# Optimization experiments

Measured on AMD Instinct MI355X. Metric: run time of the kernel, lower is better.

## Reference

```python
import jax, jax.numpy as jnp
import numpy as np

PI = float(np.pi)
TWO_PI = 2.0 * PI
LOG_2PI = float(np.log(TWO_PI))
N_FFT = 1024
LOG_N = 10
N_MAX = min(N_FFT, 2000)  # evaluate_z term cap


def _bitrev_indices(N, num_bits):
    idx = np.arange(N)
    rev = np.zeros(N, dtype=np.int32)
    v = idx.copy()
    for _ in range(num_bits):
        rev = (rev << 1) | (v & 1)
        v >>= 1
    return rev

_BITREV = jnp.asarray(_bitrev_indices(N_FFT, LOG_N))


def fft_fused(x_re, x_im):
    """Radix-2 DIT FFT with bit-reversal load, mirroring the Triton kernel.
    x_re/x_im: [B, N]. Returns (y_re, y_im)."""
    B, N = x_re.shape
    y = (x_re + 1j * x_im).astype(jnp.complex64)[:, _BITREV]
    for stage in range(LOG_N):
        s = 1 << stage          # half butterfly size (stride)
        # twiddles W_k = exp(-2*pi*i*k/(2s)), k in [0, s)
        k = jnp.arange(s)
        w = jnp.exp((-TWO_PI * 1j / (2 * s)) * k).astype(jnp.complex64)
        yg = y.reshape(B, N // (2 * s), 2, s)
        upper = yg[:, :, 0, :]
        lower = yg[:, :, 1, :] * w  # broadcast over [B, groups, s]
        y = jnp.concatenate([upper + lower, upper - lower], axis=-1).reshape(B, N)
    return jnp.real(y), jnp.imag(y)


def evaluate_z(t):
    """Riemann-Siegel Z(t) cosine sum with dynamic term count, masked."""
    t_half = t * 0.5
    theta = t_half * (jnp.log(t) - LOG_2PI) - t_half - PI / 8.0
    theta = theta + 1.0 / (48.0 * t)
    n = jnp.arange(1, N_MAX + 1, dtype=t.dtype)
    log_n = jnp.log(n)
    rsqrt_n = jax.lax.rsqrt(n)
    # [P, N_MAX] outer product of phases
    phases = t[:, None] * log_n[None, :] - theta[:, None]
    terms = rsqrt_n[None, :] * jnp.cos(phases)
    n_terms = jnp.clip(jnp.sqrt(jax.lax.stop_gradient(t) / TWO_PI).astype(jnp.int32), 10, N_MAX)
    mask = jnp.arange(N_MAX)[None, :] < n_terms[:, None]
    return 2.0 * jnp.sum(jnp.where(mask, terms, 0.0), axis=-1)


def setup_inputs() -> dict:
    key = jax.random.key(0)
    k1, k2, k3 = jax.random.split(key, 3)
    x_re = jax.random.normal(k1, (16384, N_FFT), dtype=jnp.float32)
    x_im = jax.random.normal(k2, (16384, N_FFT), dtype=jnp.float32)
    # evaluation points t in [1000, 101000)
    t = 1000.0 + 100000.0 * jax.random.uniform(k3, (262144,), dtype=jnp.float32)
    return {"x_re": x_re, "x_im": x_im, "t": t}


def reference(x_re, x_im, t):
    y_re, y_im = fft_fused(x_re, x_im)
    Z = evaluate_z(t)
    return (y_re, y_im, Z)
```

## Files before the change

### kernel.cpp

```cpp
#include <hip/hip_runtime.h>
#include <math.h>

#define INV_2PI_D 0.15915494309189535

#define LDSYNC() asm volatile("s_waitcnt lgkmcnt(0)" ::: "memory")

__device__ __forceinline__ int pad(int e) { return e + (e >> 4); }

__device__ __forceinline__ void bfly(float& ar, float& ai, float& br, float& bi,
                                     float wr, float wi) {
    const float tr = wr * br - wi * bi;
    const float ti = wr * bi + wi * br;
    br = ar - tr; bi = ai - ti;
    ar = ar + tr; ai = ai + ti;
}

__device__ __forceinline__ void wrev(float rev, float& c, float& s) {
    s = __builtin_amdgcn_sinf(rev);
    c = __builtin_amdgcn_cosf(rev);
}

__device__ __forceinline__ void fft_row(
    const float* __restrict__ xre, const float* __restrict__ xim,
    float* __restrict__ yre, float* __restrict__ yim,
    float* __restrict__ s,
    int row)
{
    const int lane = (int)(threadIdx.x & 63u);
    const size_t base = (size_t)row << 10;

    float re[16], im[16];

    const int rev6l = (int)(__brev((unsigned)lane) >> 26);
    const int REV4[16] = {0,8,4,12,2,10,6,14,1,9,5,13,3,11,7,15};
#pragma unroll
    for (int r = 0; r < 16; ++r) {
        const int a = REV4[r] * 64 + rev6l;
        re[r] = xre[base + a];
        im[r] = xim[base + a];
    }

    const int lo = lane & 15;
    const int hi = (lane >> 4) << 8;
    const float lof = (float)lo;

    float c8a[8], s8a[8];
#pragma unroll
    for (int m = 0; m < 8; ++m)
        wrev(-(16.0f * (float)m + lof) * (1.0f / 256.0f), c8a[m], s8a[m]);
    float c4a[4], s4a[4];
#pragma unroll
    for (int m = 0; m < 4; ++m)
        wrev(-(16.0f * (float)m + lof) * (1.0f / 128.0f), c4a[m], s4a[m]);
    float c2a[2], s2a[2];
#pragma unroll
    for (int m = 0; m < 2; ++m)
        wrev(-(16.0f * (float)m + lof) * (1.0f / 64.0f), c2a[m], s2a[m]);
    float c1a, s1a;
    wrev(-lof * (1.0f / 32.0f), c1a, s1a);

    const float W8R[8] = {1.f, 0.9238795325112867f, 0.7071067811865476f,
                          0.3826834323650898f, 0.f, -0.3826834323650898f,
                          -0.7071067811865476f, -0.9238795325112867f};
    const float W8I[8] = {0.f, -0.3826834323650898f, -0.7071067811865476f,
                          -0.9238795325112867f, -1.f, -0.9238795325112867f,
                          -0.7071067811865476f, -0.3826834323650898f};
#pragma unroll
    for (int st = 0; st < 4; ++st) {
        const int S = 1 << st;
#pragma unroll
        for (int rl = 0; rl < 16; ++rl) {
            if (rl & S) continue;
            const int k8 = (rl & (S - 1)) * (8 >> st);
            bfly(re[rl], im[rl], re[rl | S], im[rl | S], W8R[k8], W8I[k8]);
        }
    }

#pragma unroll
    for (int r = 0; r < 16; ++r) s[pad(lane * 16 + r)] = re[r];
    LDSYNC();
#pragma unroll
    for (int r = 0; r < 16; ++r) re[r] = s[pad(hi + (r << 4) + lo)];
    LDSYNC();
#pragma unroll
    for (int r = 0; r < 16; ++r) s[pad(lane * 16 + r)] = im[r];
    LDSYNC();
#pragma unroll
    for (int r = 0; r < 16; ++r) im[r] = s[pad(hi + (r << 4) + lo)];
    LDSYNC();

#pragma unroll
    for (int rl = 0; rl < 16; ++rl) if (!(rl & 1))
        bfly(re[rl], im[rl], re[rl|1], im[rl|1], c1a, s1a);
#pragma unroll
    for (int rl = 0; rl < 16; ++rl) if (!(rl & 2))
        bfly(re[rl], im[rl], re[rl|2], im[rl|2], c2a[rl & 1], s2a[rl & 1]);
#pragma unroll
    for (int rl = 0; rl < 16; ++rl) if (!(rl & 4))
        bfly(re[rl], im[rl], re[rl|4], im[rl|4], c4a[rl & 3], s4a[rl & 3]);
#pragma unroll
    for (int rl = 0; rl < 16; ++rl) if (!(rl & 8))
        bfly(re[rl], im[rl], re[rl|8], im[rl|8], c8a[rl & 7], s8a[rl & 7]);

    const float lf = (float)lane;
    float cz8[8], sz8[8];
#pragma unroll
    for (int m = 0; m < 8; ++m)
        wrev(-(64.0f * (float)m + lf) * (1.0f / 1024.0f), cz8[m], sz8[m]);
    float cz4[4], sz4[4];
#pragma unroll
    for (int m = 0; m < 4; ++m)
        wrev(-(64.0f * (float)m + lf) * (1.0f / 512.0f), cz4[m], sz4[m]);

#pragma unroll
    for (int r = 0; r < 16; ++r) s[pad(hi + (r << 4) + lo)] = re[r];
    LDSYNC();
#pragma unroll
    for (int r = 0; r < 16; ++r) re[r] = s[pad((r << 6) + lane)];
    LDSYNC();
#pragma unroll
    for (int r = 0; r < 16; ++r) s[pad(hi + (r << 4) + lo)] = im[r];
    LDSYNC();
#pragma unroll
    for (int r = 0; r < 16; ++r) im[r] = s[pad((r << 6) + lane)];
    LDSYNC();

#pragma unroll
    for (int rl = 0; rl < 16; ++rl) if (!(rl & 4))
        bfly(re[rl], im[rl], re[rl|4], im[rl|4], cz4[rl & 3], sz4[rl & 3]);
#pragma unroll
    for (int rl = 0; rl < 16; ++rl) if (!(rl & 8))
        bfly(re[rl], im[rl], re[rl|8], im[rl|8], cz8[rl & 7], sz8[rl & 7]);

#pragma unroll
    for (int r = 0; r < 16; ++r) {
        yre[base + (r << 6) + lane] = re[r];
        yim[base + (r << 6) + lane] = im[r];
    }
}

__global__ __launch_bounds__(256) void table_kernel(float* __restrict__ ws) {
    const int i = (int)(blockIdx.x * 256 + threadIdx.x);
    if (i < 1024) {
        const double nd = (double)(i + 1);
        ws[i]        = (float)log(nd);
        ws[1024 + i] = (float)(1.0 / sqrt(nd));
    }
}

__device__ void z_eval(const float* __restrict__ tin, float* __restrict__ zout,
                       const float* __restrict__ ws, int zblock, int n,
                       float* __restrict__ buf)
{
    for (int i = (int)threadIdx.x; i < 512; i += 256)
        reinterpret_cast<float4*>(buf)[i] = reinterpret_cast<const float4*>(ws)[i];
    __syncthreads();
    const float* slog = buf;
    const float* srsq = buf + 1024;

    const int gid = zblock * 256 + (int)threadIdx.x;
    if (gid >= n) return;

    const float t  = tin[gid];
    const float th = __fmul_rn(t, 0.5f);
    const float logt = (float)log((double)t);
    float theta = __fsub_rn(__fsub_rn(__fmul_rn(th, __fsub_rn(logt, 1.8378770664093453f)), th),
                            0.39269908169872414f);
    theta = __fadd_rn(theta, __fdiv_rn(1.0f, __fmul_rn(48.0f, t)));

    int nt = (int)sqrtf(__fdiv_rn(t, 6.283185307179586f));
    nt = min(max(nt, 10), 1024);

    float acc = 0.0f;
    for (int i = 0; i < nt; ++i) {
        const float p = __fsub_rn(__fmul_rn(t, slog[i]), theta);
        const double rev = (double)p * INV_2PI_D;
        const double fr  = rev - rint(rev);
        const float  c   = __builtin_amdgcn_cosf((float)fr);
        acc = __fmaf_rn(srsq[i], c, acc);
    }
    zout[gid] = __fmul_rn(2.0f, acc);
}

__global__ __launch_bounds__(256, 6) void fused_kernel(
    const float* __restrict__ xre, const float* __restrict__ xim,
    const float* __restrict__ tin, const float* __restrict__ ws,
    float* __restrict__ yre, float* __restrict__ yim, float* __restrict__ zout,
    int z_blocks, int nrows, int nz)
{
    __shared__ float s[4][1088];

    const int b = (int)blockIdx.x;
    if (b < z_blocks) {
        z_eval(tin, zout, ws, b, nz, &s[0][0]);
    } else {
        const int wid = (int)(threadIdx.x >> 6);
        const int row = ((b - z_blocks) << 2) | wid;
        if (row < nrows)
            fft_row(xre, xim, yre, yim, s[wid], row);
    }
}

extern "C" void kernel_launch(void* const* d_in, const int* in_sizes, int n_in,
                              void* d_out, int out_size, void* d_ws, size_t ws_size,
                              hipStream_t stream)
{
    const float* xre = (const float*)d_in[0];
    const float* xim = (const float*)d_in[1];
    const float* t   = (const float*)d_in[2];

    const size_t nfft = (size_t)in_sizes[0];
    const int nrows = (int)(nfft >> 10);
    const int nz    = in_sizes[2];

    float* yre = (float*)d_out;
    float* yim = yre + nfft;
    float* z   = yre + 2 * nfft;
    float* ws  = (float*)d_ws;

    table_kernel<<<4, 256, 0, stream>>>(ws);

    const int f_blocks = (nrows + 3) >> 2;
    const int z_blocks = (nz + 255) >> 8;
    fused_kernel<<<z_blocks + f_blocks, 256, 0, stream>>>(
        xre, xim, t, ws, yre, yim, z, z_blocks, nrows, nz);
}
```

Before: 58.12 us.

## Process two FFT rows per wavefront and compute twiddles per stage

Each wavefront now handles two FFT rows at once, so each twiddle sin/cos is computed once and shared by both rows. Twiddle generation is also moved next to the stage that uses it, which shortens register live ranges. LDS per block doubles and the occupancy hint drops from 6 to 4 blocks per CU. The aim is more independent work per wave to hide memory latency, at the cost of more registers and fewer resident waves, which also affects the co-scheduled Z-evaluation blocks.

```diff
diff --git a/kernel.cpp b/kernel.cpp
--- a/kernel.cpp
+++ b/kernel.cpp
@@ -20,44 +20,33 @@
     c = __builtin_amdgcn_cosf(rev);
 }
 
-__device__ __forceinline__ void fft_row(
+__device__ __forceinline__ void fft_rows2(
     const float* __restrict__ xre, const float* __restrict__ xim,
     float* __restrict__ yre, float* __restrict__ yim,
     float* __restrict__ s,
-    int row)
+    int row0)
 {
     const int lane = (int)(threadIdx.x & 63u);
-    const size_t base = (size_t)row << 10;
-
-    float re[16], im[16];
+
+    float re[2][16], im[2][16];
 
     const int rev6l = (int)(__brev((unsigned)lane) >> 26);
     const int REV4[16] = {0,8,4,12,2,10,6,14,1,9,5,13,3,11,7,15};
 #pragma unroll
-    for (int r = 0; r < 16; ++r) {
-        const int a = REV4[r] * 64 + rev6l;
-        re[r] = xre[base + a];
-        im[r] = xim[base + a];
+    for (int p = 0; p < 2; ++p) {
+        const size_t bb = (size_t)(row0 + p) << 10;
+        const float* xr = xre + bb + rev6l;
+        const float* xi = xim + bb + rev6l;
+#pragma unroll
+        for (int r = 0; r < 16; ++r) {
+            re[p][r] = xr[REV4[r] << 6];
+            im[p][r] = xi[REV4[r] << 6];
+        }
     }
 
     const int lo = lane & 15;
     const int hi = (lane >> 4) << 8;
     const float lof = (float)lo;
-
-    float c8a[8], s8a[8];
-#pragma unroll
-    for (int m = 0; m < 8; ++m)
-        wrev(-(16.0f * (float)m + lof) * (1.0f / 256.0f), c8a[m], s8a[m]);
-    float c4a[4], s4a[4];
-#pragma unroll
-    for (int m = 0; m < 4; ++m)
-        wrev(-(16.0f * (float)m + lof) * (1.0f / 128.0f), c4a[m], s4a[m]);
-    float c2a[2], s2a[2];
-#pragma unroll
-    for (int m = 0; m < 2; ++m)
-        wrev(-(16.0f * (float)m + lof) * (1.0f / 64.0f), c2a[m], s2a[m]);
-    float c1a, s1a;
-    wrev(-lof * (1.0f / 32.0f), c1a, s1a);
 
     const float W8R[8] = {1.f, 0.9238795325112867f, 0.7071067811865476f,
                           0.3826834323650898f, 0.f, -0.3826834323650898f,
@@ -69,38 +58,78 @@
     for (int st = 0; st < 4; ++st) {
         const int S = 1 << st;
 #pragma unroll
+        for (int p = 0; p < 2; ++p)
+#pragma unroll
         for (int rl = 0; rl < 16; ++rl) {
             if (rl & S) continue;
             const int k8 = (rl & (S - 1)) * (8 >> st);
-            bfly(re[rl], im[rl], re[rl | S], im[rl | S], W8R[k8], W8I[k8]);
+            bfly(re[p][rl], im[p][rl], re[p][rl | S], im[p][rl | S], W8R[k8], W8I[k8]);
         }
     }
 
 #pragma unroll
-    for (int r = 0; r < 16; ++r) s[pad(lane * 16 + r)] = re[r];
-    LDSYNC();
-#pragma unroll
-    for (int r = 0; r < 16; ++r) re[r] = s[pad(hi + (r << 4) + lo)];
-    LDSYNC();
-#pragma unroll
-    for (int r = 0; r < 16; ++r) s[pad(lane * 16 + r)] = im[r];
-    LDSYNC();
-#pragma unroll
-    for (int r = 0; r < 16; ++r) im[r] = s[pad(hi + (r << 4) + lo)];
-    LDSYNC();
-
-#pragma unroll
-    for (int rl = 0; rl < 16; ++rl) if (!(rl & 1))
-        bfly(re[rl], im[rl], re[rl|1], im[rl|1], c1a, s1a);
-#pragma unroll
-    for (int rl = 0; rl < 16; ++rl) if (!(rl & 2))
-        bfly(re[rl], im[rl], re[rl|2], im[rl|2], c2a[rl & 1], s2a[rl & 1]);
-#pragma unroll
-    for (int rl = 0; rl < 16; ++rl) if (!(rl & 4))
-        bfly(re[rl], im[rl], re[rl|4], im[rl|4], c4a[rl & 3], s4a[rl & 3]);
-#pragma unroll
-    for (int rl = 0; rl < 16; ++rl) if (!(rl & 8))
-        bfly(re[rl], im[rl], re[rl|8], im[rl|8], c8a[rl & 7], s8a[rl & 7]);
+    for (int p = 0; p < 2; ++p)
+#pragma unroll
+    for (int r = 0; r < 16; ++r) s[p*1088 + pad(lane * 16 + r)] = re[p][r];
+    LDSYNC();
+#pragma unroll
+    for (int p = 0; p < 2; ++p)
+#pragma unroll
+    for (int r = 0; r < 16; ++r) re[p][r] = s[p*1088 + pad(hi + (r << 4) + lo)];
+    LDSYNC();
+#pragma unroll
+    for (int p = 0; p < 2; ++p)
+#pragma unroll
+    for (int r = 0; r < 16; ++r) s[p*1088 + pad(lane * 16 + r)] = im[p][r];
+    LDSYNC();
+#pragma unroll
+    for (int p = 0; p < 2; ++p)
+#pragma unroll
+    for (int r = 0; r < 16; ++r) im[p][r] = s[p*1088 + pad(hi + (r << 4) + lo)];
+    LDSYNC();
+
+    {
+        float c1, s1;
+        wrev(-lof * (1.0f / 32.0f), c1, s1);
+#pragma unroll
+        for (int p = 0; p < 2; ++p)
+#pragma unroll
+        for (int rl = 0; rl < 16; ++rl) if (!(rl & 1))
+            bfly(re[p][rl], im[p][rl], re[p][rl|1], im[p][rl|1], c1, s1);
+    }
+    {
+        float c2[2], s2[2];
+#pragma unroll
+        for (int m = 0; m < 2; ++m)
+            wrev(-(16.0f * (float)m + lof) * (1.0f / 64.0f), c2[m], s2[m]);
+#pragma unroll
+        for (int p = 0; p < 2; ++p)
+#pragma unroll
+        for (int rl = 0; rl < 16; ++rl) if (!(rl & 2))
+            bfly(re[p][rl], im[p][rl], re[p][rl|2], im[p][rl|2], c2[rl & 1], s2[rl & 1]);
+    }
+    {
+        float c4[4], s4[4];
+#pragma unroll
+        for (int m = 0; m < 4; ++m)
+            wrev(-(16.0f * (float)m + lof) * (1.0f / 128.0f), c4[m], s4[m]);
+#pragma unroll
+        for (int p = 0; p < 2; ++p)
+#pragma unroll
+        for (int rl = 0; rl < 16; ++rl) if (!(rl & 4))
+            bfly(re[p][rl], im[p][rl], re[p][rl|4], im[p][rl|4], c4[rl & 3], s4[rl & 3]);
+    }
+    {
+        float c8[8], s8[8];
+#pragma unroll
+        for (int m = 0; m < 8; ++m)
+            wrev(-(16.0f * (float)m + lof) * (1.0f / 256.0f), c8[m], s8[m]);
+#pragma unroll
+        for (int p = 0; p < 2; ++p)
+#pragma unroll
+        for (int rl = 0; rl < 16; ++rl) if (!(rl & 8))
+            bfly(re[p][rl], im[p][rl], re[p][rl|8], im[p][rl|8], c8[rl & 7], s8[rl & 7]);
+    }
 
     const float lf = (float)lane;
     float cz8[8], sz8[8];
@@ -113,29 +142,47 @@
         wrev(-(64.0f * (float)m + lf) * (1.0f / 512.0f), cz4[m], sz4[m]);
 
 #pragma unroll
-    for (int r = 0; r < 16; ++r) s[pad(hi + (r << 4) + lo)] = re[r];
-    LDSYNC();
-#pragma unroll
-    for (int r = 0; r < 16; ++r) re[r] = s[pad((r << 6) + lane)];
-    LDSYNC();
-#pragma unroll
-    for (int r = 0; r < 16; ++r) s[pad(hi + (r << 4) + lo)] = im[r];
-    LDSYNC();
-#pragma unroll
-    for (int r = 0; r < 16; ++r) im[r] = s[pad((r << 6) + lane)];
-    LDSYNC();
-
+    for (int p = 0; p < 2; ++p)
+#pragma unroll
+    for (int r = 0; r < 16; ++r) s[p*1088 + pad(hi + (r << 4) + lo)] = re[p][r];
+    LDSYNC();
+#pragma unroll
+    for (int p = 0; p < 2; ++p)
+#pragma unroll
+    for (int r = 0; r < 16; ++r) re[p][r] = s[p*1088 + pad((r << 6) + lane)];
+    LDSYNC();
+#pragma unroll
+    for (int p = 0; p < 2; ++p)
+#pragma unroll
+    for (int r = 0; r < 16; ++r) s[p*1088 + pad(hi + (r << 4) + lo)] = im[p][r];
+    LDSYNC();
+#pragma unroll
+    for (int p = 0; p < 2; ++p)
+#pragma unroll
+    for (int r = 0; r < 16; ++r) im[p][r] = s[p*1088 + pad((r << 6) + lane)];
+    LDSYNC();
+
+#pragma unroll
+    for (int p = 0; p < 2; ++p)
 #pragma unroll
     for (int rl = 0; rl < 16; ++rl) if (!(rl & 4))
-        bfly(re[rl], im[rl], re[rl|4], im[rl|4], cz4[rl & 3], sz4[rl & 3]);
+        bfly(re[p][rl], im[p][rl], re[p][rl|4], im[p][rl|4], cz4[rl & 3], sz4[rl & 3]);
+#pragma unroll
+    for (int p = 0; p < 2; ++p)
 #pragma unroll
     for (int rl = 0; rl < 16; ++rl) if (!(rl & 8))
-        bfly(re[rl], im[rl], re[rl|8], im[rl|8], cz8[rl & 7], sz8[rl & 7]);
-
-#pragma unroll
-    for (int r = 0; r < 16; ++r) {
-        yre[base + (r << 6) + lane] = re[r];
-        yim[base + (r << 6) + lane] = im[r];
+        bfly(re[p][rl], im[p][rl], re[p][rl|8], im[p][rl|8], cz8[rl & 7], sz8[rl & 7]);
+
+#pragma unroll
+    for (int p = 0; p < 2; ++p) {
+        const size_t bb = (size_t)(row0 + p) << 10;
+        float* yr = yre + bb + lane;
+        float* yi = yim + bb + lane;
+#pragma unroll
+        for (int r = 0; r < 16; ++r) {
+            yr[r << 6] = re[p][r];
+            yi[r << 6] = im[p][r];
+        }
     }
 }
 
@@ -182,22 +229,22 @@
     zout[gid] = __fmul_rn(2.0f, acc);
 }
 
-__global__ __launch_bounds__(256, 6) void fused_kernel(
+__global__ __launch_bounds__(256, 4) void fused_kernel(
     const float* __restrict__ xre, const float* __restrict__ xim,
     const float* __restrict__ tin, const float* __restrict__ ws,
     float* __restrict__ yre, float* __restrict__ yim, float* __restrict__ zout,
     int z_blocks, int nrows, int nz)
 {
-    __shared__ float s[4][1088];
+    __shared__ float s[4][2176];
 
     const int b = (int)blockIdx.x;
     if (b < z_blocks) {
         z_eval(tin, zout, ws, b, nz, &s[0][0]);
     } else {
         const int wid = (int)(threadIdx.x >> 6);
-        const int row = ((b - z_blocks) << 2) | wid;
-        if (row < nrows)
-            fft_row(xre, xim, yre, yim, s[wid], row);
+        const int row0 = ((b - z_blocks) << 3) + (wid << 1);
+        if (row0 < nrows)
+            fft_rows2(xre, xim, yre, yim, s[wid], row0);
     }
 }
 
@@ -220,7 +267,7 @@
 
     table_kernel<<<4, 256, 0, stream>>>(ws);
 
-    const int f_blocks = (nrows + 3) >> 2;
+    const int f_blocks = (nrows + 7) >> 3;
     const int z_blocks = (nz + 255) >> 8;
     fused_kernel<<<z_blocks + f_blocks, 256, 0, stream>>>(
         xre, xim, t, ws, yre, yim, z, z_blocks, nrows, nz);
```

Result: slower. 62.01 us (+6.7%).

## Interleave Z and FFT blocks and compute log tables inside each Z block

Applied to the files above, without the earlier changes.

Z-evaluation blocks are now spread through the grid, one in every three blocks, instead of all running first. This mixes compute-bound Z work with memory-bound FFT work on each CU. The separate table-building kernel launch is removed, and each Z block computes its log and rsqrt tables into LDS with double-precision log and sqrt. This saves a launch but repeats 2048 double-precision transcendentals in every Z block. FFT load and store address arithmetic is also simplified with per-lane base pointers.

```diff
diff --git a/kernel.cpp b/kernel.cpp
--- a/kernel.cpp
+++ b/kernel.cpp
@@ -33,11 +33,12 @@
 
     const int rev6l = (int)(__brev((unsigned)lane) >> 26);
     const int REV4[16] = {0,8,4,12,2,10,6,14,1,9,5,13,3,11,7,15};
+    const float* xr = xre + base + rev6l;
+    const float* xi = xim + base + rev6l;
 #pragma unroll
     for (int r = 0; r < 16; ++r) {
-        const int a = REV4[r] * 64 + rev6l;
-        re[r] = xre[base + a];
-        im[r] = xim[base + a];
+        re[r] = xr[REV4[r] << 6];
+        im[r] = xi[REV4[r] << 6];
     }
 
     const int lo = lane & 15;
@@ -132,31 +133,26 @@
     for (int rl = 0; rl < 16; ++rl) if (!(rl & 8))
         bfly(re[rl], im[rl], re[rl|8], im[rl|8], cz8[rl & 7], sz8[rl & 7]);
 
+    float* yr = yre + base + lane;
+    float* yi = yim + base + lane;
 #pragma unroll
     for (int r = 0; r < 16; ++r) {
-        yre[base + (r << 6) + lane] = re[r];
-        yim[base + (r << 6) + lane] = im[r];
-    }
-}
-
-__global__ __launch_bounds__(256) void table_kernel(float* __restrict__ ws) {
-    const int i = (int)(blockIdx.x * 256 + threadIdx.x);
-    if (i < 1024) {
+        yr[r << 6] = re[r];
+        yi[r << 6] = im[r];
+    }
+}
+
+__device__ void z_eval(const float* __restrict__ tin, float* __restrict__ zout,
+                       int zblock, int n, float* __restrict__ buf)
+{
+    float* slog = buf;
+    float* srsq = buf + 1024;
+    for (int i = (int)threadIdx.x; i < 1024; i += 256) {
         const double nd = (double)(i + 1);
-        ws[i]        = (float)log(nd);
-        ws[1024 + i] = (float)(1.0 / sqrt(nd));
-    }
-}
-
-__device__ void z_eval(const float* __restrict__ tin, float* __restrict__ zout,
-                       const float* __restrict__ ws, int zblock, int n,
-                       float* __restrict__ buf)
-{
-    for (int i = (int)threadIdx.x; i < 512; i += 256)
-        reinterpret_cast<float4*>(buf)[i] = reinterpret_cast<const float4*>(ws)[i];
+        slog[i] = (float)log(nd);
+        srsq[i] = (float)(1.0 / sqrt(nd));
+    }
     __syncthreads();
-    const float* slog = buf;
-    const float* srsq = buf + 1024;
 
     const int gid = zblock * 256 + (int)threadIdx.x;
     if (gid >= n) return;
@@ -184,18 +180,23 @@
 
 __global__ __launch_bounds__(256, 6) void fused_kernel(
     const float* __restrict__ xre, const float* __restrict__ xim,
-    const float* __restrict__ tin, const float* __restrict__ ws,
+    const float* __restrict__ tin,
     float* __restrict__ yre, float* __restrict__ yim, float* __restrict__ zout,
     int z_blocks, int nrows, int nz)
 {
     __shared__ float s[4][1088];
 
     const int b = (int)blockIdx.x;
-    if (b < z_blocks) {
-        z_eval(tin, zout, ws, b, nz, &s[0][0]);
+    const int zi = b / 3;
+    const bool isZ = ((b % 3) == 2) && (zi < z_blocks);
+
+    if (isZ) {
+        z_eval(tin, zout, zi, nz, &s[0][0]);
     } else {
+        const int zbefore = min((b + 1) / 3, z_blocks);
+        const int fi = b - zbefore;
         const int wid = (int)(threadIdx.x >> 6);
-        const int row = ((b - z_blocks) << 2) | wid;
+        const int row = (fi << 2) | wid;
         if (row < nrows)
             fft_row(xre, xim, yre, yim, s[wid], row);
     }
@@ -216,12 +217,9 @@
     float* yre = (float*)d_out;
     float* yim = yre + nfft;
     float* z   = yre + 2 * nfft;
-    float* ws  = (float*)d_ws;
-
-    table_kernel<<<4, 256, 0, stream>>>(ws);
 
     const int f_blocks = (nrows + 3) >> 2;
     const int z_blocks = (nz + 255) >> 8;
-    fused_kernel<<<z_blocks + f_blocks, 256, 0, stream>>>(
-        xre, xim, t, ws, yre, yim, z, z_blocks, nrows, nz);
-}
+    fused_kernel<<<f_blocks + z_blocks, 256, 0, stream>>>(
+        xre, xim, t, yre, yim, z, z_blocks, nrows, nz);
+}
```

Result: faster. 54.57 us (-6.1%).
